# Kernel tuning notes

Measured on AMD Instinct MI355X. Metric: run time of the kernel, lower is better.

Reference implementation:

```python
import jax, jax.numpy as jnp
import numpy as np

XYZ_MIN = jnp.array([-1.0, -1.0, -1.0], dtype=jnp.float32)
XYZ_MAX = jnp.array([1.0, 1.0, 1.0], dtype=jnp.float32)
ACT_SHIFT = float(np.log(1.0 / (1.0 - 1e-6) - 1.0))  # density bias shift
WS = 100  # world_size per axis for num_voxels=1024000 in [-1,1]^3
R, P = 4096, 128  # rays, points per ray


def grid_sample_3d(grid, xyz):
    """Trilinear grid_sample, align_corners=True, zeros padding.
    grid: [C, D, H, W] (D=z, H=y, W=x); xyz: [N, 3] world coords. Returns [N, C]."""
    C, D, H, W = grid.shape
    norm = (xyz - XYZ_MIN) / (XYZ_MAX - XYZ_MIN) * 2.0 - 1.0  # [-1,1]
    sizes = jnp.array([W, H, D], dtype=norm.dtype)
    pix = (norm + 1.0) * 0.5 * (sizes - 1.0)  # align_corners=True mapping
    p0f = jnp.floor(pix)
    frac = pix - p0f
    p0 = p0f.astype(jnp.int32)
    out = jnp.zeros((xyz.shape[0], C), dtype=grid.dtype)
    for dx in (0, 1):
        for dy in (0, 1):
            for dz in (0, 1):
                ix, iy, iz = p0[:, 0] + dx, p0[:, 1] + dy, p0[:, 2] + dz
                wx = frac[:, 0] if dx else 1.0 - frac[:, 0]
                wy = frac[:, 1] if dy else 1.0 - frac[:, 1]
                wz = frac[:, 2] if dz else 1.0 - frac[:, 2]
                valid = ((ix >= 0) & (ix < W) & (iy >= 0) & (iy < H)
                         & (iz >= 0) & (iz < D))
                ixc = jnp.clip(ix, 0, W - 1)
                iyc = jnp.clip(iy, 0, H - 1)
                izc = jnp.clip(iz, 0, D - 1)
                vals = grid[:, izc, iyc, ixc].T  # [N, C]
                out = out + vals * (wx * wy * wz * valid)[:, None]
    return out


def setup_inputs() -> dict:
    key = jax.random.key(0)
    ks = jax.random.split(key, 12)
    origins = jax.random.uniform(ks[0], (R, 3), jnp.float32, -0.5, 0.5)
    directions = jax.random.normal(ks[1], (R, 3), jnp.float32)
    lengths = jax.random.uniform(ks[2], (R, P), jnp.float32, 0.05, 0.6)
    grid_density = jax.random.normal(ks[3], (1, WS, WS, WS), jnp.float32) * 0.1
    grid_color = jax.random.normal(ks[4], (12, WS, WS, WS), jnp.float32) * 0.1
    d_in = 12 + 27
    w1 = jax.random.normal(ks[5], (d_in, 128), jnp.float32) / np.sqrt(d_in)
    b1 = jnp.zeros((128,), jnp.float32)
    w2 = jax.random.normal(ks[6], (128, 128), jnp.float32) / np.sqrt(128)
    b2 = jnp.zeros((128,), jnp.float32)
    w3 = jax.random.normal(ks[7], (128, 3), jnp.float32) / np.sqrt(128)
    b3 = jnp.zeros((3,), jnp.float32)
    return dict(origins=origins, directions=directions, lengths=lengths,
                grid_density=grid_density, grid_color=grid_color,
                w1=w1, b1=b1, w2=w2, b2=b2, w3=w3, b3=b3)


def reference(origins, directions, lengths, grid_density, grid_color,
              w1, b1, w2, b2, w3, b3):
    # ray points: [R, P, 3]
    pts = origins[:, None, :] + directions[:, None, :] * lengths[:, :, None]
    flat = pts.reshape(-1, 3)
    # density branch
    density = grid_sample_3d(grid_density, flat).reshape(R, P, 1)
    interval = jnp.linalg.norm(directions, axis=-1)[:, None, None]
    alpha = 1.0 - (1.0 + jnp.exp(density + ACT_SHIFT)) ** (-interval)
    # color branch: 12-ch feature grid + view-dir PE + small MLP
    color = grid_sample_3d(grid_color, flat).reshape(R, P, 12)
    freqs = jnp.array([1.0, 2.0, 4.0, 8.0], dtype=jnp.float32)
    emb = (directions[:, :, None] * freqs).reshape(R, 12)
    emb = jnp.concatenate([directions, jnp.sin(emb), jnp.cos(emb)], -1)  # [R,27]
    emb = jnp.broadcast_to(emb[:, None, :], (R, P, 27))
    h = jnp.concatenate([color, emb], -1)  # [R,P,39]
    h = jax.nn.relu(h @ w1 + b1)
    h = jax.nn.relu(h @ w2 + b2)
    rgb = jax.nn.sigmoid(h @ w3 + b3)
    return alpha, rgb
```

## Files before the change

kernel.cpp:

```cpp
#include <hip/hip_runtime.h>
#include <hip/hip_bf16.h>
#include <math.h>


typedef __bf16 bf16x4 __attribute__((ext_vector_type(4)));
typedef __bf16 bf16x8 __attribute__((ext_vector_type(8)));
typedef float  f32x4  __attribute__((ext_vector_type(4)));

#define ACT_SHIFT_F (-13.815509557964774f)

#define B1R_B   45056
#define PACK2_B 2142208
#define FEAT2_B 34142208
#define NEED_FULL 46725120ull

#define EMB_B   53248
#define PACK_B  315392
#define NEED_PACK 32315392ull

__global__ __launch_bounds__(256)
void dvgo_prep2(const float* __restrict__ g_gd, const float* __restrict__ g_gc,
                const float* __restrict__ g_w1, const float* __restrict__ g_w2,
                const float* __restrict__ g_w3, const float* __restrict__ g_dir,
                const float* __restrict__ g_b1,
                bf16x8* __restrict__ pack, __bf16* __restrict__ wsb,
                float* __restrict__ b1r)
{
    const int bid = blockIdx.x;
    const int tid = threadIdx.x;
    if (bid < 3907) {
        const int gi = bid * 256 + tid;
        if (gi >= 1000000) return;
        bf16x8 v0, v1;
        #pragma unroll
        for (int c = 0; c < 8; ++c) v0[c] = (__bf16)g_gc[c * 1000000 + gi];
        #pragma unroll
        for (int c = 0; c < 4; ++c) v1[c] = (__bf16)g_gc[(8 + c) * 1000000 + gi];
        v1[4] = (__bf16)g_gd[gi];
        v1[5] = (__bf16)0.0f; v1[6] = (__bf16)0.0f; v1[7] = (__bf16)0.0f;
        pack[gi * 2 + 0] = v0;
        pack[gi * 2 + 1] = v1;
        return;
    }
    const int idx2 = bid - 3907;
    if (idx2 < 88) {
        const int idx = idx2 * 256 + tid;
        if (idx < 4096) {
            const int j = idx & 7, lane = (idx >> 3) & 63, ct = idx >> 9;
            const int n = ct * 16 + (lane & 15);
            const int k = ((lane >> 4) & 3) * 8 + j;
            wsb[idx] = (__bf16)((k < 12) ? g_w1[k * 128 + n] : 0.0f);
        } else if (idx < 20480) {
            const int i2 = idx - 4096;
            const int j = i2 & 7, lane = (i2 >> 3) & 63, ks = (i2 >> 9) & 3, ct = i2 >> 11;
            const int n = ct * 16 + (lane & 15);
            const int k = ks * 32 + ((lane >> 4) & 3) * 8 + j;
            wsb[idx] = (__bf16)g_w2[k * 128 + n];
        } else if (idx < 22528) {
            const int i3 = idx - 20480;
            const int j = i3 & 7, lane = (i3 >> 3) & 63, ks = i3 >> 9;
            const int c = lane & 15;
            const int k = ks * 32 + ((lane >> 4) & 3) * 8 + j;
            wsb[idx] = (__bf16)((c < 3) ? g_w3[k * 3 + c] : 0.0f);
        }
        return;
    }
    const int rr  = idx2 - 88;
    const int ray = rr * 2 + (tid >> 7);
    const int n   = tid & 127;
    const float d0 = g_dir[ray*3+0], d1 = g_dir[ray*3+1], d2 = g_dir[ray*3+2];
    float s = g_b1[n];
    s += d0 * g_w1[12*128 + n] + d1 * g_w1[13*128 + n] + d2 * g_w1[14*128 + n];
    #pragma unroll
    for (int m = 0; m < 12; ++m) {
        const int i = m >> 2, j = m & 3;
        const float di = (i == 0) ? d0 : ((i == 1) ? d1 : d2);
        const float a = di * (float)(1 << j);
        s += sinf(a) * g_w1[(15 + m)*128 + n];
        s += cosf(a) * g_w1[(27 + m)*128 + n];
    }
    b1r[ray*128 + n] = s;
}

__global__ __launch_bounds__(256, 6)
void dvgo_gather(const float* __restrict__ g_org, const float* __restrict__ g_dir,
                 const float* __restrict__ g_len, const bf16x8* __restrict__ pack,
                 __bf16* __restrict__ feat, float* __restrict__ out_alpha)
{
    const int pt  = blockIdx.x * 256 + threadIdx.x;
    const int ray = pt >> 7;
    const float d0 = g_dir[ray*3+0], d1 = g_dir[ray*3+1], d2 = g_dir[ray*3+2];
    const float o0 = g_org[ray*3+0], o1 = g_org[ray*3+1], o2 = g_org[ray*3+2];
    const float len = g_len[pt];

    const float px = (o0 + d0*len + 1.0f) * 49.5f;
    const float py = (o1 + d1*len + 1.0f) * 49.5f;
    const float pz = (o2 + d2*len + 1.0f) * 49.5f;
    const float fx = floorf(px), fy = floorf(py), fz = floorf(pz);
    const int ix = (int)fx, iy = (int)fy, iz = (int)fz;
    const float qx = px - fx, qy = py - fy, qz = pz - fz;
    const float wxa[2] = {1.0f - qx, qx};
    const float wya[2] = {1.0f - qy, qy};
    const float wza[2] = {1.0f - qz, qz};
    const int  cxa[2] = {min(max(ix,0),99),   min(max(ix+1,0),99)};
    const int  cya[2] = {min(max(iy,0),99),   min(max(iy+1,0),99)};
    const int  cza[2] = {min(max(iz,0),99),   min(max(iz+1,0),99)};
    const bool vxa[2] = {(unsigned)ix < 100u, (unsigned)(ix+1) < 100u};
    const bool vya[2] = {(unsigned)iy < 100u, (unsigned)(iy+1) < 100u};
    const bool vza[2] = {(unsigned)iz < 100u, (unsigned)(iz+1) < 100u};

    float den = 0.0f;
    float cc[12];
    #pragma unroll
    for (int c = 0; c < 12; ++c) cc[c] = 0.0f;

    #pragma unroll
    for (int dz = 0; dz < 2; ++dz)
    #pragma unroll
    for (int dy = 0; dy < 2; ++dy)
    #pragma unroll
    for (int dx = 0; dx < 2; ++dx) {
        float w = wxa[dx] * wya[dy] * wza[dz];
        if (!(vxa[dx] && vya[dy] && vza[dz])) w = 0.0f;
        const int gi = (cza[dz]*100 + cya[dy])*100 + cxa[dx];
        const bf16x8 v0 = pack[gi*2 + 0];
        const bf16x8 v1 = pack[gi*2 + 1];
        #pragma unroll
        for (int c = 0; c < 8; ++c) cc[c]     += w * (float)v0[c];
        #pragma unroll
        for (int c = 0; c < 4; ++c) cc[8 + c] += w * (float)v1[c];
        den += w * (float)v1[4];
    }

    const float interval = sqrtf(d0*d0 + d1*d1 + d2*d2);
    const float e = expf(den + ACT_SHIFT_F);
    out_alpha[pt] = -expm1f(-interval * log1pf(e));

    bf16x8 f0; bf16x4 f1;
    #pragma unroll
    for (int c = 0; c < 8; ++c) f0[c] = (__bf16)cc[c];
    #pragma unroll
    for (int c = 0; c < 4; ++c) f1[c] = (__bf16)cc[8 + c];
    __bf16* fo = feat + (size_t)pt * 12;
    *(bf16x8*)(fo) = f0;
    *(bf16x4*)(fo + 8) = f1;
}

__global__ __launch_bounds__(256, 4)
void dvgo_mlp(const bf16x8* __restrict__ wf, const float* __restrict__ b1r,
              const __bf16* __restrict__ feat,
              const float* __restrict__ g_b2, const float* __restrict__ g_b3,
              float* __restrict__ out_rgb)
{
    __shared__ __align__(16) char smem[32768];
    const int tid  = threadIdx.x;
    const int ray  = blockIdx.x;
    const int lane = tid & 63;
    const int wid  = tid >> 6;
    const int lr   = lane & 15;
    const int lk   = lane >> 4;
    const int sz   = (lr & 7) << 4;

    int wb1[2];
    #pragma unroll
    for (int c2 = 0; c2 < 2; ++c2)
        wb1[c2] = lr*256 + ((((wid*2 + c2)*32) + lk*8) ^ sz);
    int rb2[4];
    #pragma unroll
    for (int ks = 0; ks < 4; ++ks)
        rb2[ks] = (wid*32 + lr)*256 + ((ks*64 + lk*16) ^ sz);
    const int rowb = (wid*32 + lr)*256;

    bf16x8 zed;
    #pragma unroll
    for (int j = 0; j < 8; ++j) zed[j] = (__bf16)0.0f;

    bf16x8 aw1[2];
    #pragma unroll
    for (int c2 = 0; c2 < 2; ++c2)
        aw1[c2] = wf[(wid*2 + c2)*64 + lane];

    #pragma unroll
    for (int h = 0; h < 2; ++h) {
        bf16x8 bb[4];
        #pragma unroll
        for (int r4 = 0; r4 < 4; ++r4) {
            const int pt = ray*128 + (h*4 + r4)*16 + lr;
            const bf16x8 t0 = *(const bf16x8*)(feat + (size_t)pt*12);
            const bf16x4 t1 = *(const bf16x4*)(feat + (size_t)pt*12 + 8);
            bf16x8 tl;
            #pragma unroll
            for (int j = 0; j < 4; ++j) tl[j] = t1[j];
            #pragma unroll
            for (int j = 4; j < 8; ++j) tl[j] = (__bf16)0.0f;
            bb[r4] = (lk == 0) ? t0 : ((lk == 1) ? tl : zed);
        }
        f32x4 acc1[4][2];
        #pragma unroll
        for (int r4 = 0; r4 < 4; ++r4)
            #pragma unroll
            for (int c2 = 0; c2 < 2; ++c2) acc1[r4][c2] = (f32x4){0.f,0.f,0.f,0.f};
        #pragma unroll
        for (int r4 = 0; r4 < 4; ++r4)
            #pragma unroll
            for (int c2 = 0; c2 < 2; ++c2)
                acc1[r4][c2] = __builtin_amdgcn_mfma_f32_16x16x32_bf16(aw1[c2], bb[r4], acc1[r4][c2], 0, 0, 0);
        #pragma unroll
        for (int c2 = 0; c2 < 2; ++c2) {
            const f32x4 b1v = *(const f32x4*)(b1r + ray*128 + (wid*2 + c2)*16 + lk*4);
            #pragma unroll
            for (int r4 = 0; r4 < 4; ++r4) {
                bf16x4 hv;
                #pragma unroll
                for (int r = 0; r < 4; ++r)
                    hv[r] = (__bf16)fmaxf(acc1[r4][c2][r] + b1v[r], 0.0f);
                *(bf16x4*)(smem + wb1[c2] + (h*4 + r4)*4096) = hv;
            }
        }
    }
    __syncthreads();

    bf16x8 hq[2][4];
    #pragma unroll
    for (int q = 0; q < 2; ++q)
        #pragma unroll
        for (int ks = 0; ks < 4; ++ks)
            hq[q][ks] = *(const bf16x8*)(smem + rb2[ks] + q*4096);

    #pragma unroll
    for (int ct = 0; ct < 8; ++ct) {
        bf16x8 aw2[4];
        #pragma unroll
        for (int ks = 0; ks < 4; ++ks)
            aw2[ks] = wf[512 + (ct*4 + ks)*64 + lane];
        f32x4 a0 = (f32x4){0.f,0.f,0.f,0.f};
        f32x4 a1 = (f32x4){0.f,0.f,0.f,0.f};
        #pragma unroll
        for (int ks = 0; ks < 4; ++ks) {
            a0 = __builtin_amdgcn_mfma_f32_16x16x32_bf16(aw2[ks], hq[0][ks], a0, 0, 0, 0);
            a1 = __builtin_amdgcn_mfma_f32_16x16x32_bf16(aw2[ks], hq[1][ks], a1, 0, 0, 0);
        }
        const f32x4 b2v = *(const f32x4*)(g_b2 + ct*16 + lk*4);
        bf16x4 h0, h1;
        #pragma unroll
        for (int r = 0; r < 4; ++r) {
            h0[r] = (__bf16)fmaxf(a0[r] + b2v[r], 0.0f);
            h1[r] = (__bf16)fmaxf(a1[r] + b2v[r], 0.0f);
        }
        const int csw = (ct*32 + lk*8) ^ sz;
        *(bf16x4*)(smem + rowb + csw) = h0;
        *(bf16x4*)(smem + rowb + 4096 + csw) = h1;
    }

    bf16x8 aw3[4];
    #pragma unroll
    for (int ks = 0; ks < 4; ++ks) aw3[ks] = wf[2560 + ks*64 + lane];
    f32x4 acc3[2];
    acc3[0] = (f32x4){0.f,0.f,0.f,0.f};
    acc3[1] = (f32x4){0.f,0.f,0.f,0.f};
    #pragma unroll
    for (int q = 0; q < 2; ++q)
        #pragma unroll
        for (int ks = 0; ks < 4; ++ks) {
            const bf16x8 hq3 = *(const bf16x8*)(smem + rb2[ks] + q*4096);
            acc3[q] = __builtin_amdgcn_mfma_f32_16x16x32_bf16(aw3[ks], hq3, acc3[q], 0, 0, 0);
        }

    float* smf = (float*)(smem + wid*8192);
    if (lk == 0) {
        const float b30 = g_b3[0], b31 = g_b3[1], b32 = g_b3[2];
        #pragma unroll
        for (int q = 0; q < 2; ++q) {
            const int o = (q*16 + lr)*3;
            smf[o + 0] = 1.0f / (1.0f + __expf(-(acc3[q][0] + b30)));
            smf[o + 1] = 1.0f / (1.0f + __expf(-(acc3[q][1] + b31)));
            smf[o + 2] = 1.0f / (1.0f + __expf(-(acc3[q][2] + b32)));
        }
    }
    asm volatile("s_waitcnt lgkmcnt(0)");
    __builtin_amdgcn_sched_barrier(0);
    {
        const int base = (ray*128 + wid*32)*3;
        out_rgb[base + lane] = smf[lane];
        if (lane < 32) out_rgb[base + 64 + lane] = smf[64 + lane];
    }
}

__global__ __launch_bounds__(256)
void dvgo_prep_fb(const float* __restrict__ g_gd, const float* __restrict__ g_gc,
                  const float* __restrict__ g_w1, const float* __restrict__ g_w2,
                  const float* __restrict__ g_w3, const float* __restrict__ g_dir,
                  bf16x8* __restrict__ pack, __bf16* __restrict__ wsb, int wbase)
{
    const int bid = blockIdx.x;
    if (bid < wbase) {
        const int gi = bid * 256 + threadIdx.x;
        if (gi >= 1000000) return;
        bf16x8 v0, v1;
        #pragma unroll
        for (int c = 0; c < 8; ++c) v0[c] = (__bf16)g_gc[c * 1000000 + gi];
        #pragma unroll
        for (int c = 0; c < 4; ++c) v1[c] = (__bf16)g_gc[(8 + c) * 1000000 + gi];
        v1[4] = (__bf16)g_gd[gi];
        v1[5] = (__bf16)0.0f; v1[6] = (__bf16)0.0f; v1[7] = (__bf16)0.0f;
        pack[gi * 2 + 0] = v0;
        pack[gi * 2 + 1] = v1;
        return;
    }
    const int idx = (bid - wbase) * 256 + threadIdx.x;
    if (idx < 8192) {
        const int j = idx & 7, lane = (idx >> 3) & 63, ks = (idx >> 9) & 1, ct = idx >> 10;
        const int n = ct * 16 + (lane & 15);
        const int k = ks * 32 + ((lane >> 4) & 3) * 8 + j;
        wsb[idx] = (__bf16)((k < 39) ? g_w1[k * 128 + n] : 0.0f);
    } else if (idx < 24576) {
        const int i2 = idx - 8192;
        const int j = i2 & 7, lane = (i2 >> 3) & 63, ks = (i2 >> 9) & 3, ct = i2 >> 11;
        const int n = ct * 16 + (lane & 15);
        const int k = ks * 32 + ((lane >> 4) & 3) * 8 + j;
        wsb[idx] = (__bf16)g_w2[k * 128 + n];
    }
}

#define FB_FEAT_OFF 0
#define FB_PCC_OFF  16384
#define FB_H1_OFF   0
#define FB_PRGB_OFF 0

template <bool PACKED>
__global__ __launch_bounds__(256, 4)
void dvgo_main(const float* __restrict__ g_org, const float* __restrict__ g_dir,
               const float* __restrict__ g_len, const float* __restrict__ g_gd,
               const float* __restrict__ g_gc, const float* __restrict__ g_b1,
               const float* __restrict__ g_b2, const float* __restrict__ g_w3,
               const float* __restrict__ g_b3, const bf16x8* __restrict__ wf,
               const bf16x8* __restrict__ g_pack,
               float* __restrict__ out_alpha, float* __restrict__ out_rgb)
{
    __shared__ __align__(16) char smem[32768];
    float* smf = (float*)smem;
    const int tid = threadIdx.x;
    const int ray = blockIdx.x;
    const float d0 = g_dir[ray*3+0], d1 = g_dir[ray*3+1], d2 = g_dir[ray*3+2];
    {
        const float o0 = g_org[ray*3+0], o1 = g_org[ray*3+1], o2 = g_org[ray*3+2];
        const int p = tid & 127;
        const int dzv = tid >> 7;
        const float len = g_len[ray*128 + p];
        const float px = (o0 + d0*len + 1.0f) * 49.5f;
        const float py = (o1 + d1*len + 1.0f) * 49.5f;
        const float pz = (o2 + d2*len + 1.0f) * 49.5f;
        const float fx = floorf(px), fy = floorf(py), fz = floorf(pz);
        const int ix = (int)fx, iy = (int)fy, iz0 = (int)fz;
        const float qx = px - fx, qy = py - fy, qz = pz - fz;
        const float wxa[2] = {1.0f - qx, qx};
        const float wya[2] = {1.0f - qy, qy};
        const int  cxa[2] = {min(max(ix,0),99),   min(max(ix+1,0),99)};
        const int  cya[2] = {min(max(iy,0),99),   min(max(iy+1,0),99)};
        const bool vxa[2] = {(unsigned)ix < 100u, (unsigned)(ix+1) < 100u};
        const bool vya[2] = {(unsigned)iy < 100u, (unsigned)(iy+1) < 100u};
        const int  iz = iz0 + dzv;
        const float wz = dzv ? qz : (1.0f - qz);
        const int  cz = min(max(iz,0),99);
        const bool vz = (unsigned)iz < 100u;
        float den = 0.0f;
        float cc[12];
        #pragma unroll
        for (int c = 0; c < 12; ++c) cc[c] = 0.0f;
        #pragma unroll
        for (int dy = 0; dy < 2; ++dy)
        #pragma unroll
        for (int dx = 0; dx < 2; ++dx) {
            float w = wxa[dx] * wya[dy] * wz;
            if (!(vxa[dx] && vya[dy] && vz)) w = 0.0f;
            const int gi = (cz*100 + cya[dy])*100 + cxa[dx];
            if (PACKED) {
                const bf16x8 v0 = g_pack[gi*2 + 0];
                const bf16x8 v1 = g_pack[gi*2 + 1];
                #pragma unroll
                for (int c = 0; c < 8; ++c) cc[c]     += w * (float)v0[c];
                #pragma unroll
                for (int c = 0; c < 4; ++c) cc[8 + c] += w * (float)v1[c];
                den += w * (float)v1[4];
            } else {
                den += w * g_gd[gi];
                #pragma unroll
                for (int c = 0; c < 12; ++c) cc[c] += w * g_gc[c*1000000 + gi];
            }
        }
        if (dzv) {
            #pragma unroll
            for (int c = 0; c < 12; ++c) smf[FB_PCC_OFF/4 + p*13 + c] = cc[c];
            smf[FB_PCC_OFF/4 + p*13 + 12] = den;
        }
        __syncthreads();
        if (!dzv) {
            #pragma unroll
            for (int c = 0; c < 12; ++c) cc[c] += smf[FB_PCC_OFF/4 + p*13 + c];
            den += smf[FB_PCC_OFF/4 + p*13 + 12];
            const float interval = sqrtf(d0*d0 + d1*d1 + d2*d2);
            const float e = expf(den + ACT_SHIFT_F);
            out_alpha[ray*128 + p] = -expm1f(-interval * log1pf(e));
            bf16x8 f0; bf16x4 f1;
            #pragma unroll
            for (int c = 0; c < 8; ++c) f0[c] = (__bf16)cc[c];
            #pragma unroll
            for (int c = 0; c < 4; ++c) f1[c] = (__bf16)cc[8+c];
            const int swz = (p & 7) << 4;
            *reinterpret_cast<bf16x8*>(smem + ((FB_FEAT_OFF + p*128 +  0) ^ swz)) = f0;
            *reinterpret_cast<bf16x4*>(smem + ((FB_FEAT_OFF + p*128 + 16) ^ swz)) = f1;
        } else {
            float vals[52];
            vals[0] = d0; vals[1] = d1; vals[2] = d2;
            #pragma unroll
            for (int i = 0; i < 3; ++i) {
                const float di = (i == 0) ? d0 : ((i == 1) ? d1 : d2);
                #pragma unroll
                for (int j = 0; j < 4; ++j) {
                    const float a = di * (float)(1 << j);
                    vals[3  + i*4 + j] = sinf(a);
                    vals[15 + i*4 + j] = cosf(a);
                }
            }
            #pragma unroll
            for (int c = 27; c < 52; ++c) vals[c] = 0.0f;
            const int swz = (p & 7) << 4;
            #pragma unroll
            for (int i = 0; i < 13; ++i) {
                bf16x4 v4;
                #pragma unroll
                for (int r = 0; r < 4; ++r) v4[r] = (__bf16)vals[i*4 + r];
                *reinterpret_cast<bf16x4*>(smem + ((FB_FEAT_OFF + p*128 + 24 + i*8) ^ swz)) = v4;
            }
        }
    }
    __syncthreads();
    const int lane = tid & 63;
    const int wid  = tid >> 6;
    const int lr   = lane & 15;
    const int lk   = lane >> 4;
    {
        bf16x8 bf[2][2];
        #pragma unroll
        for (int rt = 0; rt < 2; ++rt)
            #pragma unroll
            for (int ks = 0; ks < 2; ++ks) {
                const int pt = wid*32 + rt*16 + lr;
                int a = FB_FEAT_OFF + pt*128 + ks*64 + lk*16; a ^= (pt & 7) << 4;
                bf[rt][ks] = *reinterpret_cast<const bf16x8*>(smem + a);
            }
        __syncthreads();
        f32x4 acc1[2][8];
        #pragma unroll
        for (int rt = 0; rt < 2; ++rt)
            #pragma unroll
            for (int ct = 0; ct < 8; ++ct) acc1[rt][ct] = (f32x4){0.f,0.f,0.f,0.f};
        #pragma unroll
        for (int ct = 0; ct < 8; ++ct) {
            const bf16x8 aw0 = wf[(ct*2 + 0)*64 + lane];
            const bf16x8 aw1 = wf[(ct*2 + 1)*64 + lane];
            #pragma unroll
            for (int rt = 0; rt < 2; ++rt) {
                acc1[rt][ct] = __builtin_amdgcn_mfma_f32_16x16x32_bf16(aw0, bf[rt][0], acc1[rt][ct], 0, 0, 0);
                acc1[rt][ct] = __builtin_amdgcn_mfma_f32_16x16x32_bf16(aw1, bf[rt][1], acc1[rt][ct], 0, 0, 0);
            }
        }
        #pragma unroll
        for (int ct = 0; ct < 8; ++ct) {
            const f32x4 b1v = *reinterpret_cast<const f32x4*>(g_b1 + ct*16 + lk*4);
            #pragma unroll
            for (int rt = 0; rt < 2; ++rt) {
                const int pt = wid*32 + rt*16 + lr;
                bf16x4 hv;
                #pragma unroll
                for (int r = 0; r < 4; ++r)
                    hv[r] = (__bf16)fmaxf(acc1[rt][ct][r] + b1v[r], 0.0f);
                int a = FB_H1_OFF + pt*256 + ct*32 + lk*8; a ^= (pt & 7) << 4;
                *reinterpret_cast<bf16x4*>(smem + a) = hv;
            }
        }
    }
    __syncthreads();
    const int wr = wid >> 1, wc = wid & 1;
    f32x4 acc2[4][4];
    #pragma unroll
    for (int rt = 0; rt < 4; ++rt)
        #pragma unroll
        for (int ct = 0; ct < 4; ++ct) acc2[rt][ct] = (f32x4){0.f,0.f,0.f,0.f};
    #pragma unroll
    for (int ks = 0; ks < 4; ++ks) {
        bf16x8 a2[4];
        #pragma unroll
        for (int rt = 0; rt < 4; ++rt) {
            const int pt = wr*64 + rt*16 + lr;
            int a = FB_H1_OFF + pt*256 + ks*64 + lk*16; a ^= (pt & 7) << 4;
            a2[rt] = *reinterpret_cast<const bf16x8*>(smem + a);
        }
        #pragma unroll
        for (int ct = 0; ct < 4; ++ct) {
            const int ctg = wc*4 + ct;
            const bf16x8 b2f = wf[1024 + (ctg*4 + ks)*64 + lane];
            #pragma unroll
            for (int rt = 0; rt < 4; ++rt)
                acc2[rt][ct] = __builtin_amdgcn_mfma_f32_16x16x32_bf16(a2[rt], b2f, acc2[rt][ct], 0, 0, 0);
        }
    }
    __syncthreads();
    {
        float b2v[4], w30[4], w31[4], w32[4];
        #pragma unroll
        for (int ct = 0; ct < 4; ++ct) {
            const int n2 = wc*64 + ct*16 + lr;
            b2v[ct] = g_b2[n2];
            w30[ct] = g_w3[n2*3 + 0];
            w31[ct] = g_w3[n2*3 + 1];
            w32[ct] = g_w3[n2*3 + 2];
        }
        #pragma unroll
        for (int rt = 0; rt < 4; ++rt)
            #pragma unroll
            for (int r = 0; r < 4; ++r) {
                float s0 = 0.f, s1 = 0.f, s2 = 0.f;
                #pragma unroll
                for (int ct = 0; ct < 4; ++ct) {
                    const float v = fmaxf(acc2[rt][ct][r] + b2v[ct], 0.0f);
                    s0 = fmaf(v, w30[ct], s0);
                    s1 = fmaf(v, w31[ct], s1);
                    s2 = fmaf(v, w32[ct], s2);
                }
                #pragma unroll
                for (int off = 1; off < 16; off <<= 1) {
                    s0 += __shfl_xor(s0, off);
                    s1 += __shfl_xor(s1, off);
                    s2 += __shfl_xor(s2, off);
                }
                if (lr == 0) {
                    const int pt = wr*64 + rt*16 + lk*4 + r;
                    const int base = FB_PRGB_OFF/4 + (wc*128 + pt)*3;
                    smf[base + 0] = s0;
                    smf[base + 1] = s1;
                    smf[base + 2] = s2;
                }
            }
    }
    __syncthreads();
    if (tid < 128) {
        const int p = tid;
        const float s0 = smf[p*3 + 0] + smf[(128 + p)*3 + 0] + g_b3[0];
        const float s1 = smf[p*3 + 1] + smf[(128 + p)*3 + 1] + g_b3[1];
        const float s2 = smf[p*3 + 2] + smf[(128 + p)*3 + 2] + g_b3[2];
        const int pt = ray*128 + p;
        out_rgb[pt*3 + 0] = 1.0f / (1.0f + expf(-s0));
        out_rgb[pt*3 + 1] = 1.0f / (1.0f + expf(-s1));
        out_rgb[pt*3 + 2] = 1.0f / (1.0f + expf(-s2));
    }
}

extern "C" void kernel_launch(void* const* d_in, const int* in_sizes, int n_in,
                              void* d_out, int out_size, void* d_ws, size_t ws_size,
                              hipStream_t stream)
{
    const float* g_org = (const float*)d_in[0];
    const float* g_dir = (const float*)d_in[1];
    const float* g_len = (const float*)d_in[2];
    const float* g_gd  = (const float*)d_in[3];
    const float* g_gc  = (const float*)d_in[4];
    const float* g_w1  = (const float*)d_in[5];
    const float* g_b1  = (const float*)d_in[6];
    const float* g_w2  = (const float*)d_in[7];
    const float* g_b2  = (const float*)d_in[8];
    const float* g_w3  = (const float*)d_in[9];
    const float* g_b3  = (const float*)d_in[10];
    float* out = (float*)d_out;

    if (ws_size >= NEED_FULL) {
        __bf16* wsb  = (__bf16*)d_ws;
        float*  b1r  = (float*)((char*)d_ws + B1R_B);
        bf16x8* pack = (bf16x8*)((char*)d_ws + PACK2_B);
        __bf16* feat = (__bf16*)((char*)d_ws + FEAT2_B);
        dvgo_prep2<<<6043, 256, 0, stream>>>(g_gd, g_gc, g_w1, g_w2, g_w3, g_dir,
                                             g_b1, pack, wsb, b1r);
        dvgo_gather<<<2048, 256, 0, stream>>>(g_org, g_dir, g_len, pack, feat, out);
        dvgo_mlp<<<4096, 256, 0, stream>>>((const bf16x8*)wsb, b1r, feat,
                                           g_b2, g_b3, out + 4096*128);
    } else if (ws_size >= NEED_PACK) {
        __bf16* wsb  = (__bf16*)d_ws;
        bf16x8* pack = (bf16x8*)((char*)d_ws + EMB_B);
        dvgo_prep_fb<<<4011, 256, 0, stream>>>(g_gd, g_gc, g_w1, g_w2, g_w3, g_dir,
                                               pack, wsb, 3907);
        dvgo_main<true><<<4096, 256, 0, stream>>>(g_org, g_dir, g_len, g_gd, g_gc,
                                                  g_b1, g_b2, g_w3, g_b3,
                                                  (const bf16x8*)wsb, pack,
                                                  out, out + 4096*128);
    } else {
        __bf16* wsb = (__bf16*)d_ws;
        dvgo_prep_fb<<<104, 256, 0, stream>>>(g_gd, g_gc, g_w1, g_w2, g_w3, g_dir,
                                              (bf16x8*)d_ws, wsb, 0);
        dvgo_main<false><<<4096, 256, 0, stream>>>(g_org, g_dir, g_len, g_gd, g_gc,
                                                   g_b1, g_b2, g_w3, g_b3,
                                                   (const bf16x8*)wsb, nullptr,
                                                   out, out + 4096*128);
    }
}
```

Before: 83.74 us.

## Make each wave compute its own layer-1 rows and drop the block barrier

Layer 1 was split across waves by output-column tiles, so each wave wrote part of every row into shared memory and a __syncthreads was needed before layer 2. Now each wave computes all 8 column tiles for its own 32 points and writes them to the rows it later reads itself. This removes the block-wide barrier and lets waves proceed independently. In exchange each wave loads all layer-1 weight fragments instead of two, and the barrier-free handoff depends on each wave writing and reading the same shared-memory rows.

New measurement: 83.18 us. Within noise of the previous version (-0.7%).

```diff
diff --git a/kernel.cpp b/kernel.cpp
--- a/kernel.cpp
+++ b/kernel.cpp
@@ -161,10 +161,6 @@
     const int lk   = lane >> 4;
     const int sz   = (lr & 7) << 4;
 
-    int wb1[2];
-    #pragma unroll
-    for (int c2 = 0; c2 < 2; ++c2)
-        wb1[c2] = lr*256 + ((((wid*2 + c2)*32) + lk*8) ^ sz);
     int rb2[4];
     #pragma unroll
     for (int ks = 0; ks < 4; ++ks)
@@ -175,50 +171,38 @@
     #pragma unroll
     for (int j = 0; j < 8; ++j) zed[j] = (__bf16)0.0f;
 
-    bf16x8 aw1[2];
-    #pragma unroll
-    for (int c2 = 0; c2 < 2; ++c2)
-        aw1[c2] = wf[(wid*2 + c2)*64 + lane];
-
-    #pragma unroll
-    for (int h = 0; h < 2; ++h) {
-        bf16x8 bb[4];
-        #pragma unroll
-        for (int r4 = 0; r4 < 4; ++r4) {
-            const int pt = ray*128 + (h*4 + r4)*16 + lr;
-            const bf16x8 t0 = *(const bf16x8*)(feat + (size_t)pt*12);
-            const bf16x4 t1 = *(const bf16x4*)(feat + (size_t)pt*12 + 8);
-            bf16x8 tl;
-            #pragma unroll
-            for (int j = 0; j < 4; ++j) tl[j] = t1[j];
-            #pragma unroll
-            for (int j = 4; j < 8; ++j) tl[j] = (__bf16)0.0f;
-            bb[r4] = (lk == 0) ? t0 : ((lk == 1) ? tl : zed);
-        }
-        f32x4 acc1[4][2];
-        #pragma unroll
-        for (int r4 = 0; r4 < 4; ++r4)
-            #pragma unroll
-            for (int c2 = 0; c2 < 2; ++c2) acc1[r4][c2] = (f32x4){0.f,0.f,0.f,0.f};
-        #pragma unroll
-        for (int r4 = 0; r4 < 4; ++r4)
-            #pragma unroll
-            for (int c2 = 0; c2 < 2; ++c2)
-                acc1[r4][c2] = __builtin_amdgcn_mfma_f32_16x16x32_bf16(aw1[c2], bb[r4], acc1[r4][c2], 0, 0, 0);
-        #pragma unroll
-        for (int c2 = 0; c2 < 2; ++c2) {
-            const f32x4 b1v = *(const f32x4*)(b1r + ray*128 + (wid*2 + c2)*16 + lk*4);
-            #pragma unroll
-            for (int r4 = 0; r4 < 4; ++r4) {
-                bf16x4 hv;
-                #pragma unroll
-                for (int r = 0; r < 4; ++r)
-                    hv[r] = (__bf16)fmaxf(acc1[r4][c2][r] + b1v[r], 0.0f);
-                *(bf16x4*)(smem + wb1[c2] + (h*4 + r4)*4096) = hv;
-            }
-        }
-    }
-    __syncthreads();
+    bf16x8 bb[2];
+    #pragma unroll
+    for (int q = 0; q < 2; ++q) {
+        const int pt = ray*128 + wid*32 + q*16 + lr;
+        const bf16x8 t0 = *(const bf16x8*)(feat + (size_t)pt*12);
+        const bf16x4 t1 = *(const bf16x4*)(feat + (size_t)pt*12 + 8);
+        bf16x8 tl;
+        #pragma unroll
+        for (int j = 0; j < 4; ++j) tl[j] = t1[j];
+        #pragma unroll
+        for (int j = 4; j < 8; ++j) tl[j] = (__bf16)0.0f;
+        bb[q] = (lk == 0) ? t0 : ((lk == 1) ? tl : zed);
+    }
+
+    #pragma unroll
+    for (int ct = 0; ct < 8; ++ct) {
+        const bf16x8 aw = wf[ct*64 + lane];
+        f32x4 a0 = (f32x4){0.f,0.f,0.f,0.f};
+        f32x4 a1 = (f32x4){0.f,0.f,0.f,0.f};
+        a0 = __builtin_amdgcn_mfma_f32_16x16x32_bf16(aw, bb[0], a0, 0, 0, 0);
+        a1 = __builtin_amdgcn_mfma_f32_16x16x32_bf16(aw, bb[1], a1, 0, 0, 0);
+        const f32x4 b1v = *(const f32x4*)(b1r + ray*128 + ct*16 + lk*4);
+        bf16x4 h0, h1;
+        #pragma unroll
+        for (int r = 0; r < 4; ++r) {
+            h0[r] = (__bf16)fmaxf(a0[r] + b1v[r], 0.0f);
+            h1[r] = (__bf16)fmaxf(a1[r] + b1v[r], 0.0f);
+        }
+        const int csw = (ct*32 + lk*8) ^ sz;
+        *(bf16x4*)(smem + rowb + csw) = h0;
+        *(bf16x4*)(smem + rowb + 4096 + csw) = h1;
+    }
 
     bf16x8 hq[2][4];
     #pragma unroll
```
